# Kernel tuning notes

Hardware: AMD Instinct MI355X
Metric: run time of the kernel (lower is better)

## Reference

```python
import jax, jax.numpy as jnp
import numpy as np

B, C, H, W = 16, 64, 256, 256
STRIDE = 2
IN_KS = 3
OUT_KS = 3  # must be odd
HP, WP = H // STRIDE, W // STRIDE


def setup_inputs() -> dict:
    key = jax.random.key(0)
    k1, k2, k3 = jax.random.split(key, 3)
    f = jax.random.normal(k1, (B, C, HP, WP), dtype=jnp.float32)
    # Provenance: for pooled cell (i, j), the argmax location within the
    # IN_KS x IN_KS window anchored at (i*STRIDE, j*STRIDE), as a flat h*w index.
    dy = jax.random.randint(k2, (B, C, HP, WP), 0, IN_KS)
    dx = jax.random.randint(k3, (B, C, HP, WP), 0, IN_KS)
    rows = jnp.clip(jnp.arange(HP)[None, None, :, None] * STRIDE + dy, 0, H - 1)
    cols = jnp.clip(jnp.arange(WP)[None, None, None, :] * STRIDE + dx, 0, W - 1)
    provenance = (rows * W + cols).astype(jnp.int32)
    return {"f": f, "provenance": provenance, "h": H, "w": W}


def reference(f, provenance, h, w):
    b, c, hp, wp = f.shape
    # --- unpool: scatter pooled values to provenance locations in an h*w canvas ---
    vals = f.reshape(b * c, hp * wp)
    idx = provenance.reshape(b * c, hp * wp)
    scatter = lambda i, v: jnp.zeros((h * w,), f.dtype).at[i].set(v)
    up = jax.vmap(scatter)(idx, vals).reshape(b, c, h, w)
    # --- dilation: OUT_KS x OUT_KS windowed max, stride 1, 'same' padding ---
    p = (OUT_KS - 1) // 2
    out = jax.lax.reduce_window(
        up, -jnp.inf, jax.lax.max,
        window_dimensions=(1, 1, OUT_KS, OUT_KS),
        window_strides=(1, 1, 1, 1),
        padding=[(0, 0), (0, 0), (p, p), (p, p)],
    )
    return out
```

## Files before the change

### kernel.cpp

```cpp
#include <hip/hip_runtime.h>
#include <math.h>

#define BATCH 16
#define CHAN  64
#define Hh    256
#define Ww    256
#define HP    128
#define WP    128
#define TH    64
#define TW    64
#define CH    66
#define CW    66
#define CS    68

typedef unsigned int u32;
typedef float vfloat4 __attribute__((ext_vector_type(4)));

__global__ __launch_bounds__(256, 8) void unpool_dilate_kernel(
    const float* __restrict__ f, const int* __restrict__ prov,
    float* __restrict__ out)
{
    __shared__ __align__(16) u32 s[CH * CS];

    const int tid = threadIdx.x;
    const int bc  = blockIdx.y;
    const int ty  = blockIdx.x >> 2;
    const int tx  = blockIdx.x & 3;
    const int y0  = ty * TH;
    const int x0  = tx * TW;

    const int pi_min = (ty == 0) ? 0 : (ty * 32 - 1);
    const int pj_min = (tx == 0) ? 0 : (tx * 32 - 1);
    const int pi_max = min(HP - 1, ty * 32 + 32);
    const int pj_max = min(WP - 1, tx * 32 + 32);
    const size_t in_base = (size_t)bc * (HP * WP);

    u32   m_key[5];
    float m_f[5];
    int   m_p[5];
    bool  m_v[5];
    #pragma unroll
    for (int it = 0; it < 5; ++it) {
        const int k  = tid + it * 256;
        const int ki = k / 34;
        const int kj = k - ki * 34;
        m_v[it] = (k < 34 * 34) & (pi_min + ki <= pi_max) & (pj_min + kj <= pj_max);
        const int pi = min(pi_min + ki, pi_max);
        const int pj = min(pj_min + kj, pj_max);
        const int q  = pi * WP + pj;
        m_key[it] = (u32)(q + 1);
        m_p[it]   = prov[in_base + q];
        m_f[it]   = f[in_base + q];
    }

    {
        uint4* p4 = (uint4*)s;
        const uint4 z = make_uint4(0u, 0u, 0u, 0u);
        #pragma unroll
        for (int it = 0; it < 5; ++it) {
            const int idx = tid + it * 256;
            if (idx < (CH * CS) / 4) p4[idx] = z;
        }
    }
    const u32 NEGINF = 0xFF800000u;
    if (ty == 0 && tid < CW) s[tid] = NEGINF;
    if (ty == 3 && tid < CW) s[(CH - 1) * CS + tid] = NEGINF;
    if (tx == 0 && tid < CH) s[tid * CS] = NEGINF;
    if (tx == 3 && tid < CH) s[tid * CS + (CW - 1)] = NEGINF;
    __syncthreads();

    int m_li[5];
    #pragma unroll
    for (int it = 0; it < 5; ++it) {
        const int p  = m_p[it];
        const int lr = (p >> 8) - y0 + 1;
        const int lc = (p & 255) - x0 + 1;
        if (m_v[it] && (unsigned)lr < CH && (unsigned)lc < CW) {
            const int li = lr * CS + lc;
            m_li[it] = li;
            atomicMax(&s[li], m_key[it]);
        } else {
            m_li[it] = -1;
        }
    }
    __syncthreads();

    #pragma unroll
    for (int it = 0; it < 5; ++it) {
        if (m_li[it] >= 0 && s[m_li[it]] == m_key[it])
            s[m_li[it]] = __float_as_uint(m_f[it]);
    }
    __syncthreads();

    const float* sf = (const float*)s;
    const int tr = tid >> 4;
    const int tc = tid & 15;
    const int r0 = 4 * tr;
    const int c0 = 4 * tc;

    float h0[4], h1[4];
    const size_t obase = (size_t)bc * (Hh * Ww) + (size_t)(y0 + r0) * Ww + (x0 + c0);

    #pragma unroll
    for (int r = 0; r < 6; ++r) {
        const float* row = sf + (r0 + r) * CS + c0;
        const float4 a = *(const float4*)row;
        const float2 b = *(const float2*)(row + 4);
        float h[4];
        h[0] = fmaxf(fmaxf(a.x, a.y), a.z);
        h[1] = fmaxf(fmaxf(a.y, a.z), a.w);
        h[2] = fmaxf(fmaxf(a.z, a.w), b.x);
        h[3] = fmaxf(fmaxf(a.w, b.x), b.y);
        if (r >= 2) {
            vfloat4 res;
            res.x = fmaxf(fmaxf(h0[0], h1[0]), h[0]);
            res.y = fmaxf(fmaxf(h0[1], h1[1]), h[1]);
            res.z = fmaxf(fmaxf(h0[2], h1[2]), h[2]);
            res.w = fmaxf(fmaxf(h0[3], h1[3]), h[3]);
            __builtin_nontemporal_store(res, (vfloat4*)(out + obase + (size_t)(r - 2) * Ww));
        }
        #pragma unroll
        for (int j = 0; j < 4; ++j) { h0[j] = h1[j]; h1[j] = h[j]; }
    }
}

extern "C" void kernel_launch(void* const* d_in, const int* in_sizes, int n_in,
                              void* d_out, int out_size, void* d_ws, size_t ws_size,
                              hipStream_t stream) {
    const float* f    = (const float*)d_in[0];
    const int*   prov = (const int*)d_in[1];
    float* out = (float*)d_out;

    dim3 grid((Hh / TH) * (Ww / TW), BATCH * CHAN);
    unpool_dilate_kernel<<<grid, 256, 0, stream>>>(f, prov, out);
}
```

Before: 364.3 us.

## Use full-width row-strip tiles with 1024-thread blocks to cut halo reloads

Each block now covers a 64x256 full-width strip instead of a 64x64 tile, so horizontal halos disappear and the candidate input reads become contiguous full rows. Block size goes from 256 to 1024 threads and shared memory grows to about 69KB. The -inf border initialisation is folded into the zero-fill. This trades less redundant input loading and simpler indexing for lower occupancy per CU and larger barrier groups.

After: 371.2 us. Within noise of the previous version (+1.9%).

```diff
diff --git a/kernel.cpp b/kernel.cpp
--- a/kernel.cpp
+++ b/kernel.cpp
@@ -8,79 +8,79 @@
 #define HP    128
 #define WP    128
 #define TH    64
-#define TW    64
-#define CH    66
-#define CW    66
-#define CS    68
+#define CHs   66
+#define CWs   258
+#define S     260
+#define NW4   (CHs * (S / 4))
+#define NCAND (34 * 128)
 
 typedef unsigned int u32;
 typedef float vfloat4 __attribute__((ext_vector_type(4)));
 
-__global__ __launch_bounds__(256, 8) void unpool_dilate_kernel(
+__global__ __launch_bounds__(1024, 8) void unpool_dilate_kernel(
     const float* __restrict__ f, const int* __restrict__ prov,
     float* __restrict__ out)
 {
-    __shared__ __align__(16) u32 s[CH * CS];
+    __shared__ __align__(16) u32 s[CHs * S];
 
     const int tid = threadIdx.x;
+    const int ty  = blockIdx.x;
     const int bc  = blockIdx.y;
-    const int ty  = blockIdx.x >> 2;
-    const int tx  = blockIdx.x & 3;
     const int y0  = ty * TH;
-    const int x0  = tx * TW;
-
-    const int pi_min = (ty == 0) ? 0 : (ty * 32 - 1);
-    const int pj_min = (tx == 0) ? 0 : (tx * 32 - 1);
-    const int pi_max = min(HP - 1, ty * 32 + 32);
-    const int pj_max = min(WP - 1, tx * 32 + 32);
     const size_t in_base = (size_t)bc * (HP * WP);
 
+    const int pi0 = ty * 32 - 1;
     u32   m_key[5];
+    int   m_p[5];
     float m_f[5];
-    int   m_p[5];
-    bool  m_v[5];
     #pragma unroll
     for (int it = 0; it < 5; ++it) {
-        const int k  = tid + it * 256;
-        const int ki = k / 34;
-        const int kj = k - ki * 34;
-        m_v[it] = (k < 34 * 34) & (pi_min + ki <= pi_max) & (pj_min + kj <= pj_max);
-        const int pi = min(pi_min + ki, pi_max);
-        const int pj = min(pj_min + kj, pj_max);
-        const int q  = pi * WP + pj;
-        m_key[it] = (u32)(q + 1);
-        m_p[it]   = prov[in_base + q];
-        m_f[it]   = f[in_base + q];
+        const int k = tid + it * 1024;
+        m_key[it] = 0;
+        if (k < NCAND) {
+            const int ki = k >> 7;
+            const int kj = k & 127;
+            const int pi = min(max(pi0 + ki, 0), HP - 1);
+            const int q  = (pi << 7) + kj;
+            m_key[it] = (u32)(q + 1);
+            m_p[it]   = prov[in_base + q];
+            m_f[it]   = f[in_base + q];
+        }
     }
 
     {
+        const u32 NI = 0xFF800000u;
         uint4* p4 = (uint4*)s;
-        const uint4 z = make_uint4(0u, 0u, 0u, 0u);
         #pragma unroll
         for (int it = 0; it < 5; ++it) {
-            const int idx = tid + it * 256;
-            if (idx < (CH * CS) / 4) p4[idx] = z;
+            const int idx = tid + it * 1024;
+            if (idx < NW4) {
+                const int row = idx / 65;
+                const int c4  = (idx - row * 65) * 4;
+                const bool rinf = (ty == 0 && row == 0) | (ty == 3 && row == CHs - 1);
+                uint4 v;
+                v.x = (rinf | (c4 == 0))   ? NI : 0u;
+                v.y = (rinf | (c4 == 256)) ? NI : 0u;
+                v.z = rinf ? NI : 0u;
+                v.w = rinf ? NI : 0u;
+                p4[idx] = v;
+            }
         }
     }
-    const u32 NEGINF = 0xFF800000u;
-    if (ty == 0 && tid < CW) s[tid] = NEGINF;
-    if (ty == 3 && tid < CW) s[(CH - 1) * CS + tid] = NEGINF;
-    if (tx == 0 && tid < CH) s[tid * CS] = NEGINF;
-    if (tx == 3 && tid < CH) s[tid * CS + (CW - 1)] = NEGINF;
     __syncthreads();
 
     int m_li[5];
     #pragma unroll
     for (int it = 0; it < 5; ++it) {
-        const int p  = m_p[it];
-        const int lr = (p >> 8) - y0 + 1;
-        const int lc = (p & 255) - x0 + 1;
-        if (m_v[it] && (unsigned)lr < CH && (unsigned)lc < CW) {
-            const int li = lr * CS + lc;
-            m_li[it] = li;
-            atomicMax(&s[li], m_key[it]);
-        } else {
-            m_li[it] = -1;
+        m_li[it] = -1;
+        if (m_key[it]) {
+            const int p  = m_p[it];
+            const int lr = (p >> 8) - y0 + 1;
+            if ((unsigned)lr < CHs) {
+                const int li = lr * S + (p & 255) + 1;
+                m_li[it] = li;
+                atomicMax(&s[li], m_key[it]);
+            }
         }
     }
     __syncthreads();
@@ -93,17 +93,16 @@
     __syncthreads();
 
     const float* sf = (const float*)s;
-    const int tr = tid >> 4;
-    const int tc = tid & 15;
-    const int r0 = 4 * tr;
+    const int tr = tid >> 6;
+    const int tc = tid & 63;
     const int c0 = 4 * tc;
 
     float h0[4], h1[4];
-    const size_t obase = (size_t)bc * (Hh * Ww) + (size_t)(y0 + r0) * Ww + (x0 + c0);
+    const size_t obase = (size_t)bc * (Hh * Ww) + (size_t)(y0 + 4 * tr) * Ww + c0;
 
     #pragma unroll
     for (int r = 0; r < 6; ++r) {
-        const float* row = sf + (r0 + r) * CS + c0;
+        const float* row = sf + (4 * tr + r) * S + c0;
         const float4 a = *(const float4*)row;
         const float2 b = *(const float2*)(row + 4);
         float h[4];
@@ -131,6 +130,6 @@
     const int*   prov = (const int*)d_in[1];
     float* out = (float*)d_out;
 
-    dim3 grid((Hh / TH) * (Ww / TW), BATCH * CHAN);
-    unpool_dilate_kernel<<<grid, 256, 0, stream>>>(f, prov, out);
+    dim3 grid(Hh / TH, BATCH * CHAN);
+    unpool_dilate_kernel<<<grid, 1024, 0, stream>>>(f, prov, out);
 }
```
